# Optimization experiments

Hardware: AMD Instinct MI355X
Metric: run time of the kernel (lower is better)

The kernel has to match this reference:

```python
import jax, jax.numpy as jnp
import numpy as np

EMBED_DIM = 64  # matches init_kwargs embed_dim; used for 1/sqrt(d) scaling


def setup_inputs() -> dict:
    key = jax.random.key(0)
    k1, k2, k3, k4 = jax.random.split(key, 4)
    N1, N2, C, B = 8192, 8192, EMBED_DIM, 8
    query = jax.random.normal(k1, (N1, C), dtype=jnp.float32)
    key_value = jax.random.normal(k2, (N2, C), dtype=jnp.float32)
    # sorted batch indices so per-batch concat order == input row order
    query_coors = jnp.sort(jax.random.randint(k3, (N1,), 0, B))
    key_value_coors = jnp.sort(jax.random.randint(k4, (N2,), 0, B))
    return {
        "query": query,
        "key_value": key_value,
        "query_coors": query_coors,
        "key_value_coors": key_value_coors,
    }


def reference(query, key_value, query_coors, key_value_coors):
    # Per-batch attention: each query row attends only to key_value rows with
    # the same batch index. Equivalent to the original per-batch loop +
    # chunked softmax(QK^T/sqrt(d)) V, expressed as one masked attention.
    # Dropout is identity (eval mode) for a deterministic correctness baseline.
    scale = 1.0 / jnp.sqrt(jnp.asarray(EMBED_DIM, dtype=query.dtype))
    scores = jnp.einsum("nc,mc->nm", query, key_value) * scale  # [N1, N2]
    same_batch = query_coors[:, None] == key_value_coors[None, :]
    neg_inf = jnp.asarray(-jnp.inf, dtype=scores.dtype)
    scores = jnp.where(same_batch, scores, neg_inf)
    attn = jax.nn.softmax(scores, axis=-1)  # softmax within each batch segment
    out = jnp.einsum("nm,mc->nc", attn, key_value)  # [N1, C]
    return out
```

## Files before the change

kernel.cpp:

```cpp
#include <hip/hip_runtime.h>
#include <hip/hip_bf16.h>

typedef __attribute__((ext_vector_type(8))) short bf16x8;
typedef __attribute__((ext_vector_type(4))) unsigned short u16x4;
typedef __attribute__((ext_vector_type(8))) unsigned short u16x8;
typedef __attribute__((ext_vector_type(4))) float f32x4;

#define NEG_INF (-__builtin_inff())
#define QSCALE (0.125f * 1.4426950408889634f)
#define CONST_M 12.0f
#define NC 8
#define NCL2 3

#define SWZK(a) ((a) ^ ((((((a) >> 7) & 3) | ((((a) >> 10) & 1) << 2)) << 4)))

static __device__ __forceinline__ unsigned short f2bf(float x) {
  union { float f; unsigned u; } v; v.f = x;
  unsigned r = (v.u + 0x7fffu + ((v.u >> 16) & 1u)) >> 16;
  return (unsigned short)r;
}
static __device__ __forceinline__ float bf2f(unsigned short h) {
  union { unsigned u; float f; } v; v.u = ((unsigned)h) << 16;
  return v.f;
}

__global__ __launch_bounds__(256) void prep_kv_kernel(
    const float* __restrict__ kv, const int* __restrict__ kvc,
    unsigned short* __restrict__ kvb, unsigned short* __restrict__ kvt,
    int* __restrict__ seg, int nkv) {
  __shared__ unsigned short tile[16][64];
  const int nb8 = gridDim.x >> 3;
  const int bp = ((gridDim.x & 7) == 0) ? ((blockIdx.x & 7) * nb8 + (blockIdx.x >> 3))
                                        : blockIdx.x;
  const int rowbase = bp * 16;
  const int t = threadIdx.x;
  if (t < 16) {
    int i = rowbase + t;
    if (i < nkv) {
      int c = kvc[i];
      int cp = (i == 0) ? -1 : kvc[i - 1];
      if (c != cp) {
        for (int b = cp + 1; b <= c; ++b) seg[b] = i;
        if (i == 0) for (int b = 0; b < c; ++b) seg[8 + b] = 0;
      }
      int cn = (i == nkv - 1) ? 8 : kvc[i + 1];
      if (c != cn) {
        for (int b = c; b < cn; ++b) seg[8 + b] = i + 1;
        if (i == nkv - 1) for (int b = c + 1; b < 8; ++b) seg[b] = nkv;
      }
    }
  }
  const int r = t >> 4;
  const int c = (t & 15) * 4;
  float4 a = *(const float4*)(kv + (size_t)(rowbase + r) * 64 + c);
  u16x4 v4;
  v4[0] = f2bf(a.x); v4[1] = f2bf(a.y); v4[2] = f2bf(a.z); v4[3] = f2bf(a.w);
  *(u16x4*)(kvb + (size_t)(rowbase + r) * 64 + c) = v4;
  *(u16x4*)&tile[r][c] = v4;
  __syncthreads();
  const int d = t & 63;
  const int k0 = (t >> 6) * 4;
  u16x4 wv;
#pragma unroll
  for (int j = 0; j < 4; ++j) wv[j] = tile[k0 + j][d];
  const int blk = rowbase >> 5;
  const int kbase = (rowbase & 31) + k0;
  *(u16x4*)(kvt + (size_t)blk * 2048 + d * 32 + kbase) = wv;
}

#define STAGE_LOAD(kvx)                                                        \
  {                                                                            \
    const int kvL_ = (kvx);                                                    \
    const char* src_ = stK ? ((const char*)kvb + (size_t)kvL_ * 128 + soff)    \
                           : ((const char*)kvt + (((size_t)kvL_) >> 5) * 4096 + soff); \
    sreg = *(const f32x4*)src_;                                                \
  }
#define STAGE_WRITE(BUF) { *(f32x4*)(ldsbuf[BUF] + doff) = sreg; }

#define STEP(BUF, kvx)                                                         \
  {                                                                            \
    const int kv0_ = (kvx);                                                    \
    const char* Lb_ = ldsbuf[BUF];                                             \
    bf16x8 kf0_ = *(const bf16x8*)(Lb_ + koff0);                               \
    bf16x8 kf1_ = *(const bf16x8*)(Lb_ + koff1);                               \
    bf16x8 kf2_ = *(const bf16x8*)(Lb_ + koff2);                               \
    bf16x8 kf3_ = *(const bf16x8*)(Lb_ + koff3);                               \
    bf16x8 vf0_ = *(const bf16x8*)(Lb_ + voff0);                               \
    bf16x8 vf1_ = *(const bf16x8*)(Lb_ + voff1);                               \
    bf16x8 vf2_ = *(const bf16x8*)(Lb_ + voff2);                               \
    bf16x8 vf3_ = *(const bf16x8*)(Lb_ + voff3);                               \
    f32x4 z_ = {0, 0, 0, 0};                                                   \
    __builtin_amdgcn_s_setprio(1);                                             \
    f32x4 sT0 = __builtin_amdgcn_mfma_f32_16x16x32_bf16(kf0_, qf0, z_, 0, 0, 0); \
    sT0 = __builtin_amdgcn_mfma_f32_16x16x32_bf16(kf1_, qf1, sT0, 0, 0, 0);    \
    f32x4 sT1 = __builtin_amdgcn_mfma_f32_16x16x32_bf16(kf2_, qf0, z_, 0, 0, 0); \
    sT1 = __builtin_amdgcn_mfma_f32_16x16x32_bf16(kf3_, qf1, sT1, 0, 0, 0);    \
    __builtin_amdgcn_s_setprio(0);                                             \
    float v_[8];                                                               \
    const bool full_ = uniformb && (kv0_ >= kv_lo) && (kv0_ + 32 <= kv_hi);    \
    if (full_) {                                                               \
      _Pragma("unroll") for (int r = 0; r < 4; ++r) {                          \
        v_[r] = sT0[r]; v_[4 + r] = sT1[r];                                    \
      }                                                                        \
    } else {                                                                   \
      const int kb0_ = kv0_ + g8;                                              \
      _Pragma("unroll") for (int r = 0; r < 4; ++r) {                          \
        v_[r]     = (kb0_ + r     >= lo_q && kb0_ + r     < hi_q) ? sT0[r] : NEG_INF; \
        v_[4 + r] = (kb0_ + r + 4 >= lo_q && kb0_ + r + 4 < hi_q) ? sT1[r] : NEG_INF; \
      }                                                                        \
    }                                                                          \
    float t_ = fmaxf(fmaxf(fmaxf(v_[0], v_[1]), fmaxf(v_[2], v_[3])),          \
                     fmaxf(fmaxf(v_[4], v_[5]), fmaxf(v_[6], v_[7])));         \
    if (__builtin_expect(__any(t_ > m), 0)) {                                  \
      float tt_ = fmaxf(t_, __shfl_xor(t_, 16));                               \
      tt_ = fmaxf(tt_, __shfl_xor(tt_, 32));                                   \
      float mn_ = fmaxf(m, tt_);                                               \
      float f_ = __builtin_exp2f(m - mn_);                                     \
      l *= f_;                                                                 \
      _Pragma("unroll") for (int r = 0; r < 4; ++r) {                          \
        acc0[r] *= f_; acc1[r] *= f_; acc2[r] *= f_; acc3[r] *= f_;            \
      }                                                                        \
      m = mn_;                                                                 \
    }                                                                          \
    float e_[8];                                                               \
    _Pragma("unroll") for (int i = 0; i < 8; ++i)                              \
      e_[i] = __builtin_exp2f(v_[i] - m);                                      \
    l += (((e_[0] + e_[1]) + (e_[2] + e_[3])) +                                \
          ((e_[4] + e_[5]) + (e_[6] + e_[7])));                                \
    bf16x8 pa_;                                                                \
    _Pragma("unroll") for (int j = 0; j < 8; ++j) pa_[j] = (short)f2bf(e_[j]); \
    __builtin_amdgcn_s_setprio(1);                                             \
    acc0 = __builtin_amdgcn_mfma_f32_16x16x32_bf16(vf0_, pa_, acc0, 0, 0, 0);  \
    acc1 = __builtin_amdgcn_mfma_f32_16x16x32_bf16(vf1_, pa_, acc1, 0, 0, 0);  \
    acc2 = __builtin_amdgcn_mfma_f32_16x16x32_bf16(vf2_, pa_, acc2, 0, 0, 0);  \
    acc3 = __builtin_amdgcn_mfma_f32_16x16x32_bf16(vf3_, pa_, acc3, 0, 0, 0);  \
    __builtin_amdgcn_s_setprio(0);                                             \
  }

__global__ __launch_bounds__(512, 4) void attn_kernel(
    const float* __restrict__ qf,
    const unsigned short* __restrict__ kvb,
    const unsigned short* __restrict__ kvt,
    const int* __restrict__ qc,
    const int* __restrict__ seg,
    unsigned short* __restrict__ pacc,
    float2* __restrict__ pml,
    int n2)
{
  __shared__ __attribute__((aligned(16))) char ldsbuf[2][8192];

  const int per8 = gridDim.x >> 3;
  const int ii = ((gridDim.x & 7) == 0) ? ((blockIdx.x & 7) * per8 + (blockIdx.x >> 3))
                                        : blockIdx.x;
  const int qt = ii >> NCL2;
  const int c  = ii & (NC - 1);
  const int qbase = qt << 7;

  const int tid = threadIdx.x;
  const int w = tid >> 6;
  const int lane = tid & 63;
  const int q16 = lane & 15;
  const int g = lane >> 4;
  const int g8 = g * 8;
  const int q0w = qbase + w * 16;

  const bool stK = tid < 256;
  const int soff = (tid & 255) * 16;
  const int doff = stK ? SWZK(soff) : 4096 + soff;
  f32x4 sreg;

  const int myb = qc[q0w + q16];
  const int lo_q = seg[myb];
  const int hi_q = seg[8 + myb];
  const int bfirst = qc[qbase];
  const int blast  = qc[qbase + 127];
  const int kv_lo  = seg[bfirst];
  const int kv_hi  = seg[8 + blast];
  const bool uniformb = (bfirst == blast);

  bf16x8 qf0, qf1;
  {
    const float* qr = qf + (size_t)(q0w + q16) * 64 + g8;
    float4 a0 = *(const float4*)(qr),      a1 = *(const float4*)(qr + 4);
    float4 a2 = *(const float4*)(qr + 32), a3 = *(const float4*)(qr + 36);
    qf0[0]=(short)f2bf(a0.x*QSCALE); qf0[1]=(short)f2bf(a0.y*QSCALE);
    qf0[2]=(short)f2bf(a0.z*QSCALE); qf0[3]=(short)f2bf(a0.w*QSCALE);
    qf0[4]=(short)f2bf(a1.x*QSCALE); qf0[5]=(short)f2bf(a1.y*QSCALE);
    qf0[6]=(short)f2bf(a1.z*QSCALE); qf0[7]=(short)f2bf(a1.w*QSCALE);
    qf1[0]=(short)f2bf(a2.x*QSCALE); qf1[1]=(short)f2bf(a2.y*QSCALE);
    qf1[2]=(short)f2bf(a2.z*QSCALE); qf1[3]=(short)f2bf(a2.w*QSCALE);
    qf1[4]=(short)f2bf(a3.x*QSCALE); qf1[5]=(short)f2bf(a3.y*QSCALE);
    qf1[6]=(short)f2bf(a3.z*QSCALE); qf1[7]=(short)f2bf(a3.w*QSCALE);
  }

  const int base = kv_lo & ~31;
  const int nblk = (kv_hi - base + 31) >> 5;
  const int b0i = (nblk * c) >> NCL2;
  const int b1i = (nblk * (c + 1)) >> NCL2;

  const int rowoff = ((q16 >> 2) << 3) + (q16 & 3);
  const int koff0 = SWZK(rowoff * 128 + g * 16);
  const int koff1 = SWZK(rowoff * 128 + 64 + g * 16);
  const int koff2 = SWZK((rowoff + 4) * 128 + g * 16);
  const int koff3 = SWZK((rowoff + 4) * 128 + 64 + g * 16);
  const int voff0 = 4096 + (q16 +  0) * 64 + g * 16;
  const int voff1 = 4096 + (q16 + 16) * 64 + g * 16;
  const int voff2 = 4096 + (q16 + 32) * 64 + g * 16;
  const int voff3 = 4096 + (q16 + 48) * 64 + g * 16;

  f32x4 acc0 = {0,0,0,0}, acc1 = {0,0,0,0}, acc2 = {0,0,0,0}, acc3 = {0,0,0,0};
  float m = CONST_M;
  float l = 0.0f;

  if (b0i < b1i) {
    STAGE_LOAD(base + b0i * 32);
    STAGE_WRITE(0);
    __syncthreads();
    int cur = 0;
    for (int b = b0i; b < b1i; ++b) {
      const bool more = (b + 1 < b1i);
      if (more) STAGE_LOAD(base + (b + 1) * 32);
      STEP(cur, base + b * 32);
      if (more) STAGE_WRITE(cur ^ 1);
      __syncthreads();
      cur ^= 1;
    }
  }

  l += __shfl_xor(l, 16);
  l += __shfl_xor(l, 32);

  const int row = q0w + q16;
  unsigned short* pr = pacc + ((size_t)row * NC + c) * 64;
  u16x4 h0, h1, h2, h3;
#pragma unroll
  for (int r = 0; r < 4; ++r) {
    h0[r] = f2bf(acc0[r]); h1[r] = f2bf(acc1[r]);
    h2[r] = f2bf(acc2[r]); h3[r] = f2bf(acc3[r]);
  }
  *(u16x4*)(pr + 0  + g * 4) = h0;
  *(u16x4*)(pr + 16 + g * 4) = h1;
  *(u16x4*)(pr + 32 + g * 4) = h2;
  *(u16x4*)(pr + 48 + g * 4) = h3;
  if (g == 0) {
    float2 v; v.x = m; v.y = l;
    pml[(size_t)row * NC + c] = v;
  }
}

__global__ __launch_bounds__(256) void merge_kernel(
    const unsigned short* __restrict__ pacc, const float2* __restrict__ pml,
    float* __restrict__ out)
{
  const int nb8 = gridDim.x >> 3;
  const int bq = ((gridDim.x & 7) == 0) ? ((blockIdx.x & 7) * nb8 + (blockIdx.x >> 3))
                                        : blockIdx.x;
  const int q0 = bq * 16;
  const int t = threadIdx.x;
  const int i = t >> 4;
  const int c0 = (t & 15) * 4;
  const int R = q0 + i;

  float mm[NC], ll[NC], sc[NC];
  float mstar = NEG_INF;
#pragma unroll
  for (int cc = 0; cc < NC; ++cc) {
    float2 v = pml[(size_t)R * NC + cc];
    mm[cc] = v.x; ll[cc] = v.y;
    mstar = fmaxf(mstar, v.x);
  }
  float L = 0.0f;
#pragma unroll
  for (int cc = 0; cc < NC; ++cc) {
    sc[cc] = __builtin_exp2f(mm[cc] - mstar);
    L += sc[cc] * ll[cc];
  }
  float inv = (L > 0.0f) ? 1.0f / L : 0.0f;
  f32x4 num = {0, 0, 0, 0};
#pragma unroll
  for (int cc = 0; cc < NC; ++cc) {
    u16x4 a = *(const u16x4*)&pacc[((size_t)R * NC + cc) * 64 + c0];
    float s = sc[cc];
    num[0] += s * bf2f(a[0]); num[1] += s * bf2f(a[1]);
    num[2] += s * bf2f(a[2]); num[3] += s * bf2f(a[3]);
  }
  f32x4 o;
  o[0] = num[0] * inv; o[1] = num[1] * inv;
  o[2] = num[2] * inv; o[3] = num[3] * inv;
  *(f32x4*)&out[(size_t)R * 64 + c0] = o;
}

extern "C" void kernel_launch(void* const* d_in, const int* in_sizes, int n_in,
                              void* d_out, int out_size, void* d_ws, size_t ws_size,
                              hipStream_t stream) {
  const float* q  = (const float*)d_in[0];
  const float* kv = (const float*)d_in[1];
  const int* qc   = (const int*)d_in[2];
  const int* kvc  = (const int*)d_in[3];
  float* out = (float*)d_out;

  const int C = 64;
  const int n1 = in_sizes[0] / C;
  const int n2 = in_sizes[1] / C;

  char* ws = (char*)d_ws;
  size_t off = 0;
  unsigned short* kvb = (unsigned short*)(ws + off); off += (size_t)n2 * C * 2;
  unsigned short* kvt = (unsigned short*)(ws + off); off += (size_t)n2 * C * 2;
  int* seg = (int*)(ws + off); off += 4096;
  unsigned short* pacc = (unsigned short*)(ws + off); off += (size_t)n1 * NC * 64 * 2;
  float2* pml = (float2*)(ws + off);

  prep_kv_kernel<<<n2 / 16, 256, 0, stream>>>(kv, kvc, kvb, kvt, seg, n2);
  attn_kernel<<<(n1 / 128) * NC, 512, 0, stream>>>(q, kvb, kvt, qc, seg, pacc, pml, n2);
  merge_kernel<<<n1 / 16, 256, 0, stream>>>(pacc, pml, out);
}
```

Measured before the change: 26.30 us.

## Fuse KV bf16 conversion and segment search into attention kernel

Removes the separate prep kernel that converted key/value rows to bf16 (plus a transposed copy) and computed batch segment bounds. The attention kernel now loads fp32 KV straight from global memory, converts to bf16 while staging into LDS, and writes V transposed with scalar stores. Segment bounds come from per-thread binary searches over the sorted coordinate array. This saves a kernel launch and a workspace round trip, but doubles the global bytes read per KV tile, repeats the conversion in every block, and adds scattered LDS writes plus the search latency.

```diff
diff --git a/kernel.cpp b/kernel.cpp
--- a/kernel.cpp
+++ b/kernel.cpp
@@ -24,58 +24,26 @@
   return v.f;
 }
 
-__global__ __launch_bounds__(256) void prep_kv_kernel(
-    const float* __restrict__ kv, const int* __restrict__ kvc,
-    unsigned short* __restrict__ kvb, unsigned short* __restrict__ kvt,
-    int* __restrict__ seg, int nkv) {
-  __shared__ unsigned short tile[16][64];
-  const int nb8 = gridDim.x >> 3;
-  const int bp = ((gridDim.x & 7) == 0) ? ((blockIdx.x & 7) * nb8 + (blockIdx.x >> 3))
-                                        : blockIdx.x;
-  const int rowbase = bp * 16;
-  const int t = threadIdx.x;
-  if (t < 16) {
-    int i = rowbase + t;
-    if (i < nkv) {
-      int c = kvc[i];
-      int cp = (i == 0) ? -1 : kvc[i - 1];
-      if (c != cp) {
-        for (int b = cp + 1; b <= c; ++b) seg[b] = i;
-        if (i == 0) for (int b = 0; b < c; ++b) seg[8 + b] = 0;
-      }
-      int cn = (i == nkv - 1) ? 8 : kvc[i + 1];
-      if (c != cn) {
-        for (int b = c; b < cn; ++b) seg[8 + b] = i + 1;
-        if (i == nkv - 1) for (int b = c + 1; b < 8; ++b) seg[b] = nkv;
-      }
-    }
-  }
-  const int r = t >> 4;
-  const int c = (t & 15) * 4;
-  float4 a = *(const float4*)(kv + (size_t)(rowbase + r) * 64 + c);
-  u16x4 v4;
-  v4[0] = f2bf(a.x); v4[1] = f2bf(a.y); v4[2] = f2bf(a.z); v4[3] = f2bf(a.w);
-  *(u16x4*)(kvb + (size_t)(rowbase + r) * 64 + c) = v4;
-  *(u16x4*)&tile[r][c] = v4;
-  __syncthreads();
-  const int d = t & 63;
-  const int k0 = (t >> 6) * 4;
-  u16x4 wv;
-#pragma unroll
-  for (int j = 0; j < 4; ++j) wv[j] = tile[k0 + j][d];
-  const int blk = rowbase >> 5;
-  const int kbase = (rowbase & 31) + k0;
-  *(u16x4*)(kvt + (size_t)blk * 2048 + d * 32 + kbase) = wv;
-}
-
 #define STAGE_LOAD(kvx)                                                        \
   {                                                                            \
-    const int kvL_ = (kvx);                                                    \
-    const char* src_ = stK ? ((const char*)kvb + (size_t)kvL_ * 128 + soff)    \
-                           : ((const char*)kvt + (((size_t)kvL_) >> 5) * 4096 + soff); \
-    sreg = *(const f32x4*)src_;                                                \
-  }
-#define STAGE_WRITE(BUF) { *(f32x4*)(ldsbuf[BUF] + doff) = sreg; }
+    const float* s_ = kvf + ((size_t)((kvx) + sr)) * 64 + sc0;                 \
+    sA = *(const float4*)s_;                                                   \
+    sB = *(const float4*)(s_ + 4);                                             \
+  }
+
+#define STAGE_WRITE(BUF)                                                       \
+  {                                                                            \
+    float xs_[8] = {sA.x, sA.y, sA.z, sA.w, sB.x, sB.y, sB.z, sB.w};           \
+    if (stK) {                                                                 \
+      u16x8 h_;                                                                \
+      _Pragma("unroll") for (int e = 0; e < 8; ++e) h_[e] = f2bf(xs_[e]);      \
+      *(u16x8*)(ldsbuf[BUF] + kdst) = h_;                                      \
+    } else {                                                                   \
+      unsigned short* vb_ = (unsigned short*)(ldsbuf[BUF] + 4096);             \
+      _Pragma("unroll") for (int e = 0; e < 8; ++e)                            \
+        vb_[(sc0 + e) * 32 + sr] = f2bf(xs_[e]);                               \
+    }                                                                          \
+  }
 
 #define STEP(BUF, kvx)                                                         \
   {                                                                            \
@@ -139,10 +107,9 @@
 
 __global__ __launch_bounds__(512, 4) void attn_kernel(
     const float* __restrict__ qf,
-    const unsigned short* __restrict__ kvb,
-    const unsigned short* __restrict__ kvt,
+    const float* __restrict__ kvf,
     const int* __restrict__ qc,
-    const int* __restrict__ seg,
+    const int* __restrict__ kvc,
     unsigned short* __restrict__ pacc,
     float2* __restrict__ pml,
     int n2)
@@ -165,18 +132,11 @@
   const int q0w = qbase + w * 16;
 
   const bool stK = tid < 256;
-  const int soff = (tid & 255) * 16;
-  const int doff = stK ? SWZK(soff) : 4096 + soff;
-  f32x4 sreg;
-
-  const int myb = qc[q0w + q16];
-  const int lo_q = seg[myb];
-  const int hi_q = seg[8 + myb];
-  const int bfirst = qc[qbase];
-  const int blast  = qc[qbase + 127];
-  const int kv_lo  = seg[bfirst];
-  const int kv_hi  = seg[8 + blast];
-  const bool uniformb = (bfirst == blast);
+  const int tt = tid & 255;
+  const int sr  = tt >> 3;
+  const int sc0 = (tt & 7) * 8;
+  const int kdst = SWZK(sr * 128 + sc0 * 2);
+  float4 sA, sB;
 
   bf16x8 qf0, qf1;
   {
@@ -193,6 +153,21 @@
     qf1[6]=(short)f2bf(a3.z*QSCALE); qf1[7]=(short)f2bf(a3.w*QSCALE);
   }
 
+  const int myb    = qc[q0w + q16];
+  const int bfirst = qc[qbase];
+  const int blast  = qc[qbase + 127];
+  const bool uniformb = (bfirst == blast);
+  int lA = 0, hA = n2, lB = 0, hB = n2, lC = 0, hC = n2, lD = 0, hD = n2;
+#pragma unroll 1
+  for (int it = 0; it < 14; ++it) {
+    if (lA < hA) { int m_ = (lA + hA) >> 1; if (kvc[m_] <  myb)    lA = m_ + 1; else hA = m_; }
+    if (lB < hB) { int m_ = (lB + hB) >> 1; if (kvc[m_] <= myb)    lB = m_ + 1; else hB = m_; }
+    if (lC < hC) { int m_ = (lC + hC) >> 1; if (kvc[m_] <  bfirst) lC = m_ + 1; else hC = m_; }
+    if (lD < hD) { int m_ = (lD + hD) >> 1; if (kvc[m_] <= blast)  lD = m_ + 1; else hD = m_; }
+  }
+  const int lo_q = hA, hi_q = hB;
+  const int kv_lo = hC, kv_hi = hD;
+
   const int base = kv_lo & ~31;
   const int nblk = (kv_hi - base + 31) >> 5;
   const int b0i = (nblk * c) >> NCL2;
@@ -305,13 +280,9 @@
 
   char* ws = (char*)d_ws;
   size_t off = 0;
-  unsigned short* kvb = (unsigned short*)(ws + off); off += (size_t)n2 * C * 2;
-  unsigned short* kvt = (unsigned short*)(ws + off); off += (size_t)n2 * C * 2;
-  int* seg = (int*)(ws + off); off += 4096;
   unsigned short* pacc = (unsigned short*)(ws + off); off += (size_t)n1 * NC * 64 * 2;
   float2* pml = (float2*)(ws + off);
 
-  prep_kv_kernel<<<n2 / 16, 256, 0, stream>>>(kv, kvc, kvb, kvt, seg, n2);
-  attn_kernel<<<(n1 / 128) * NC, 512, 0, stream>>>(q, kvb, kvt, qc, seg, pacc, pml, n2);
+  attn_kernel<<<(n1 / 128) * NC, 512, 0, stream>>>(q, kv, qc, kvc, pacc, pml, n2);
   merge_kernel<<<n1 / 16, 256, 0, stream>>>(pacc, pml, out);
 }
```

After: 28.77 us. 9.4% more time.
